# Kernel tuning notes

Hardware: AMD Instinct MI355X
Metric: run time of the kernel (lower is better)

The kernel has to match this reference:

```python
import jax, jax.numpy as jnp
import numpy as np

BLOCK = 256
H, D = 16, 128          # num_attention_heads, head_dim
HID = 2048              # hidden_size (= H*D)
FFN = 2048              # intermediate_size
E, TOPK = 8, 2          # num_local_experts, num_experts_per_tok
EPS_LN = 1e-5           # rms_norm_eps for layer norms
EPS_ATTN = float(np.finfo(np.float32).eps)  # torch RMSNorm default eps


def rmsnorm(x, w, eps):
    v = jnp.mean(jnp.square(x), axis=-1, keepdims=True)
    return x * jax.lax.rsqrt(v + eps) * w


def lightning_attn(x, slope, qkv_w, gate_w, norm_w, out_w):
    # x: [B,N,HID]; slope: [H,1,1]
    B, N, _ = x.shape
    qkv = jax.nn.silu(x @ qkv_w.T).reshape(B, N, H, 3 * D)
    q, k, v = jnp.split(qkv, 3, axis=-1)
    q = q.transpose(0, 2, 1, 3)  # [B,H,N,D]
    k = k.transpose(0, 2, 1, 3)
    v = v.transpose(0, 2, 1, 3)

    NB = N // BLOCK
    ar = jnp.arange(BLOCK, dtype=jnp.float32) + 1.0
    q_decay = jnp.exp(-slope * ar[:, None])             # [H,BLOCK,1]
    k_decay = jnp.exp(-slope * (BLOCK - ar[:, None]))   # [H,BLOCK,1]
    idx = ar[:, None] - ar[None, :]                      # [BLOCK,BLOCK]
    diag_decay = jnp.exp(jnp.where(idx >= 0, -(slope * idx), -jnp.inf))  # [H,BLOCK,BLOCK]
    block_decay = jnp.exp(-slope * BLOCK)                # [H,1,1]

    qb = q.reshape(B, H, NB, BLOCK, D).transpose(2, 0, 1, 3, 4)  # [NB,B,H,BLOCK,D]
    kb = k.reshape(B, H, NB, BLOCK, D).transpose(2, 0, 1, 3, 4)
    vb = v.reshape(B, H, NB, BLOCK, D).transpose(2, 0, 1, 3, 4)

    def step(kv, blk):
        qi, ki, vi = blk                                   # [B,H,BLOCK,D]
        o_nd = jnp.einsum('bhmd,bhde->bhme', qi * q_decay, kv)
        qk = jnp.einsum('bhmd,bhnd->bhmn', qi, ki) * diag_decay[None]
        o_d = jnp.einsum('bhmn,bhne->bhme', qk, vi)
        kv = block_decay * kv + jnp.einsum('bhmd,bhme->bhde', ki * k_decay, vi)
        return kv, o_nd + o_d

    kv0 = jnp.zeros((B, H, D, D), jnp.float32)
    _, out = jax.lax.scan(step, kv0, (qb, kb, vb))         # out: [NB,B,H,BLOCK,D]
    out = out.transpose(1, 2, 0, 3, 4).reshape(B, H, N, D)
    out = out.transpose(0, 2, 1, 3).reshape(B, N, H * D)   # b h n d -> b n (h d)
    out = rmsnorm(out, norm_w, EPS_ATTN)
    out = jax.nn.sigmoid(x @ gate_w.T) * out
    return out @ out_w.T


def moe(x, router_w, w1, w2, w3):
    # x: [B,N,HID]
    B, N, _ = x.shape
    xt = x.reshape(B * N, HID)                             # [T,HID]
    T = B * N
    logits = xt @ router_w.T                               # [T,E]
    probs = jax.nn.softmax(logits.astype(jnp.float32), axis=-1)
    w, sel = jax.lax.top_k(probs, TOPK)                    # [T,TOPK]
    w = w / jnp.sum(w, axis=-1, keepdims=True)
    w = w.astype(xt.dtype)
    # dense combine weights [T,E] (top-k experts are distinct)
    cw = jnp.zeros((T, E), xt.dtype).at[jnp.arange(T)[:, None], sel].add(w)
    h1 = jax.nn.silu(jnp.einsum('td,efd->tef', xt, w1))    # [T,E,FFN]
    h3 = jnp.einsum('td,efd->tef', xt, w3)
    ye = jnp.einsum('tef,edf->ted', h1 * h3, w2)           # [T,E,HID]
    out = jnp.einsum('te,ted->td', cw, ye)
    return out.reshape(B, N, HID)


def setup_inputs() -> dict:
    key = jax.random.key(0)
    ks = jax.random.split(key, 12)
    s = 0.02
    B, N = 1, 1024
    x = jax.random.normal(ks[0], (B, N, HID), jnp.float32)
    # ALiBi-like positive per-head decay rates
    slope_rate = (1.0 / (2.0 ** (8.0 * (jnp.arange(H, dtype=jnp.float32) + 1) / H))).reshape(H, 1, 1)
    return {
        'x': x,
        'slope_rate': slope_rate,
        'ln1_w': jnp.ones((HID,), jnp.float32),
        'ln2_w': jnp.ones((HID,), jnp.float32),
        'qkv_w': jax.random.normal(ks[1], (3 * H * D, HID), jnp.float32) * s,
        'ogate_w': jax.random.normal(ks[2], (H * D, HID), jnp.float32) * s,
        'anorm_w': jnp.ones((H * D,), jnp.float32),
        'aout_w': jax.random.normal(ks[3], (HID, H * D), jnp.float32) * s,
        'router_w': jax.random.normal(ks[4], (E, HID), jnp.float32) * s,
        'w1': jax.random.normal(ks[5], (E, FFN, HID), jnp.float32) * s,
        'w2': jax.random.normal(ks[6], (E, HID, FFN), jnp.float32) * s,
        'w3': jax.random.normal(ks[7], (E, FFN, HID), jnp.float32) * s,
    }


def reference(x, slope_rate, ln1_w, ln2_w, qkv_w, ogate_w, anorm_w, aout_w, router_w, w1, w2, w3):
    # pre-norm residual decoder layer (alpha=beta=1, postnorm=False, no shared MoE)
    r = x
    h = rmsnorm(x, ln1_w, EPS_LN)
    h = r + lightning_attn(h, slope_rate, qkv_w, ogate_w, anorm_w, aout_w)
    r = h
    h2 = rmsnorm(h, ln2_w, EPS_LN)
    return r + moe(h2, router_w, w1, w2, w3)
```

## Files before the change

kernel.cpp:

```cpp
#include <hip/hip_runtime.h>
#include <math.h>

#define NTOK 1024
#define NHID 2048
#define NQKV 6144
#define NHEADS 16
#define DHEAD 128
#define ABLK 256
#define NEXPERT 8
#define NFFN 2048
#define EPS_LN 1e-5f
#define EPS_ATTN 1.1920929e-7f

typedef __bf16 bf8v __attribute__((ext_vector_type(8)));
typedef __bf16 bf4v __attribute__((ext_vector_type(4)));
typedef float f4v __attribute__((ext_vector_type(4)));

static __device__ __forceinline__ f4v mfma16(bf8v a, bf8v b, f4v c) {
  return __builtin_amdgcn_mfma_f32_16x16x32_bf16(a, b, c, 0, 0, 0);
}

static __device__ __forceinline__ void gl2lds16(const void* g, void* l) {
  __builtin_amdgcn_global_load_lds(
      (const __attribute__((address_space(1))) unsigned int*)g,
      (__attribute__((address_space(3))) unsigned int*)l, 16, 0, 0);
}

__global__ __launch_bounds__(256) void rms_kernel(const float* __restrict__ in,
                                                  const float* __restrict__ w,
                                                  __bf16* __restrict__ out_bf,
                                                  const float* __restrict__ gate,
                                                  float* __restrict__ copy_out,
                                                  float* __restrict__ out_f32,
                                                  float eps) {
  const int row = blockIdx.x, tid = threadIdx.x;
  const float* p = in + (size_t)row * NHID;
  float4 v0 = *(const float4*)(p + 4 * tid);
  float4 v1 = *(const float4*)(p + 1024 + 4 * tid);
  float ss = v0.x * v0.x + v0.y * v0.y + v0.z * v0.z + v0.w * v0.w
           + v1.x * v1.x + v1.y * v1.y + v1.z * v1.z + v1.w * v1.w;
  for (int off = 32; off > 0; off >>= 1) ss += __shfl_down(ss, off);
  __shared__ float red[4];
  const int wv = tid >> 6, ln = tid & 63;
  if (ln == 0) red[wv] = ss;
  __syncthreads();
  const float tot = red[0] + red[1] + red[2] + red[3];
  const float rinv = rsqrtf(tot * (1.f / NHID) + eps);
  float4 w0 = *(const float4*)(w + 4 * tid);
  float4 w1 = *(const float4*)(w + 1024 + 4 * tid);
  float4 o0, o1;
  o0.x = v0.x * rinv * w0.x; o0.y = v0.y * rinv * w0.y;
  o0.z = v0.z * rinv * w0.z; o0.w = v0.w * rinv * w0.w;
  o1.x = v1.x * rinv * w1.x; o1.y = v1.y * rinv * w1.y;
  o1.z = v1.z * rinv * w1.z; o1.w = v1.w * rinv * w1.w;
  if (gate) {
    const float* gp = gate + (size_t)row * NHID;
    float4 g0 = *(const float4*)(gp + 4 * tid);
    float4 g1 = *(const float4*)(gp + 1024 + 4 * tid);
    o0.x *= g0.x; o0.y *= g0.y; o0.z *= g0.z; o0.w *= g0.w;
    o1.x *= g1.x; o1.y *= g1.y; o1.z *= g1.z; o1.w *= g1.w;
  }
  bf4v b0, b1;
  b0[0] = (__bf16)o0.x; b0[1] = (__bf16)o0.y; b0[2] = (__bf16)o0.z; b0[3] = (__bf16)o0.w;
  b1[0] = (__bf16)o1.x; b1[1] = (__bf16)o1.y; b1[2] = (__bf16)o1.z; b1[3] = (__bf16)o1.w;
  *(bf4v*)(out_bf + (size_t)row * NHID + 4 * tid) = b0;
  *(bf4v*)(out_bf + (size_t)row * NHID + 1024 + 4 * tid) = b1;
  if (out_f32) {
    *(float4*)(out_f32 + (size_t)row * NHID + 4 * tid) = o0;
    *(float4*)(out_f32 + (size_t)row * NHID + 1024 + 4 * tid) = o1;
  }
  if (copy_out) {
    *(float4*)(copy_out + (size_t)row * NHID + 4 * tid) = v0;
    *(float4*)(copy_out + (size_t)row * NHID + 1024 + 4 * tid) = v1;
  }
}

enum { GM_QKV = 0, GM_GATE = 1, GM_AOUT = 2, GM_MOE1 = 3, GM_MOE3 = 4, GM_MOE2 = 5 };

struct GArgs {
  const __bf16* A; const float* B; void* C;
  const float* res;
  __bf16* q_s; __bf16* k_s; __bf16* v_s;
  const int* perm; const int* segoff; const float* pw;
  float* outp;
  int N, K;
};

template <int MODE>
__global__ __launch_bounds__(256, 3) void gemm_bt(GArgs g) {
  const int n0 = blockIdx.x * 64;
  const int m0 = blockIdx.y * 128;
  int segbase = 0, cnt = 0x40000000, e = 0;
  if constexpr (MODE >= GM_MOE1) {
    e = blockIdx.z;
    segbase = g.segoff[e];
    cnt = g.segoff[e + 1] - segbase;
    if (m0 >= cnt) return;
  }
  const float* Bp = g.B + (size_t)e * g.N * g.K + (size_t)n0 * g.K;
  __shared__ __bf16 As[3][128 * 32] __attribute__((aligned(16)));
  __shared__ float Bs[3][64 * 32] __attribute__((aligned(16)));
  const int tid = threadIdx.x;
  const int w = tid >> 6, lane = tid & 63;
  const int wm = (w >> 1) * 64, wn = (w & 1) * 32;
  const int lm = lane & 15, quad = lane >> 4;
  const int K = g.K;

  const __bf16* aptr[2];
#pragma unroll
  for (int qi = 0; qi < 2; qi++) {
    const int r = w * 32 + qi * 16 + (lane >> 2);
    const int m = m0 + r;
    long grow;
    if constexpr (MODE == GM_MOE1 || MODE == GM_MOE3) {
      int mm = m < cnt ? m : cnt - 1;
      grow = g.perm[segbase + mm];
    } else if constexpr (MODE == GM_MOE2) {
      grow = segbase + (m < cnt ? m : cnt - 1);
    } else {
      grow = m;
    }
    const int gc = (lane & 3) ^ (r & 3);
    aptr[qi] = g.A + (size_t)grow * K + gc * 8;
  }
  const float* bptr[2];
  {
    const int lr = lane >> 3;
    const int coff = ((lane & 7) ^ lr) * 4;
#pragma unroll
    for (int qi = 0; qi < 2; qi++) {
      const int r = (w * 2 + qi) * 8 + lr;
      bptr[qi] = Bp + (size_t)r * K + coff;
    }
  }

  const f4v fz = {0.f, 0.f, 0.f, 0.f};
  f4v acc[4][2];
#pragma unroll
  for (int i = 0; i < 4; i++) {
    acc[i][0] = fz; acc[i][1] = fz;
  }

  const int KT = K >> 5;

#define STAGE(tt, bb)                                      \
  do {                                                     \
    const int kk_ = (tt) << 5;                             \
    gl2lds16(aptr[0] + kk_, &As[bb][(w * 32) * 32]);       \
    gl2lds16(aptr[1] + kk_, &As[bb][(w * 32 + 16) * 32]);  \
    gl2lds16(bptr[0] + kk_, &Bs[bb][(w * 16) * 32]);       \
    gl2lds16(bptr[1] + kk_, &Bs[bb][(w * 16 + 8) * 32]);   \
  } while (0)

  STAGE(0, 0);
  STAGE(1, 1);

  const int swa = lm & 3;
  const int swb = lm & 7;
  for (int t = 0; t < KT; ++t) {
    const int cur = t % 3;
    if (t + 1 < KT) {
      asm volatile("s_waitcnt vmcnt(4)" ::: "memory");
    } else {
      asm volatile("s_waitcnt vmcnt(0)" ::: "memory");
    }
    __builtin_amdgcn_s_barrier();
    if (t + 2 < KT) {
      const int nb = (t + 2) % 3;
      STAGE(t + 2, nb);
    }
    bf8v af[4], bfv[2];
#pragma unroll
    for (int i = 0; i < 4; i++) {
      const int ra = wm + i * 16 + lm;
      af[i] = *(const bf8v*)&As[cur][ra * 32 + ((quad ^ swa) << 3)];
    }
#pragma unroll
    for (int j = 0; j < 2; j++) {
      const int rb = wn + j * 16 + lm;
      const float4 x0 = *(const float4*)&Bs[cur][rb * 32 + (((quad * 2) ^ swb) << 2)];
      const float4 x1 = *(const float4*)&Bs[cur][rb * 32 + (((quad * 2 + 1) ^ swb) << 2)];
      bf8v t8;
      t8[0] = (__bf16)x0.x; t8[1] = (__bf16)x0.y; t8[2] = (__bf16)x0.z; t8[3] = (__bf16)x0.w;
      t8[4] = (__bf16)x1.x; t8[5] = (__bf16)x1.y; t8[6] = (__bf16)x1.z; t8[7] = (__bf16)x1.w;
      bfv[j] = t8;
    }
#pragma unroll
    for (int i = 0; i < 4; i++)
#pragma unroll
      for (int j = 0; j < 2; j++) acc[i][j] = mfma16(af[i], bfv[j], acc[i][j]);
  }
#undef STAGE

#pragma unroll
  for (int i = 0; i < 4; i++) {
#pragma unroll
    for (int r = 0; r < 4; r++) {
      const int m = m0 + wm + i * 16 + quad * 4 + r;
      int tok = 0;
      float wgt = 0.f;
      if constexpr (MODE == GM_MOE2) {
        if (m < cnt) { tok = g.perm[segbase + m]; wgt = g.pw[segbase + m]; }
      }
#pragma unroll
      for (int j = 0; j < 2; j++) {
        const int col = n0 + wn + j * 16 + lm;
        float v = acc[i][j][r];
        if constexpr (MODE == GM_QKV) {
          v = v / (1.f + expf(-v));
          int head = col / 384;
          int rem = col - head * 384;
          int which = rem >> 7;
          int d = rem & 127;
          __bf16* dst = which == 0 ? g.q_s : (which == 1 ? g.k_s : g.v_s);
          dst[((size_t)head * NTOK + m) * DHEAD + d] = (__bf16)v;
        } else if constexpr (MODE == GM_GATE) {
          ((float*)g.C)[(size_t)m * g.N + col] = 1.f / (1.f + expf(-v));
        } else if constexpr (MODE == GM_AOUT) {
          ((float*)g.C)[(size_t)m * g.N + col] = v + g.res[(size_t)m * g.N + col];
        } else if constexpr (MODE == GM_MOE1) {
          if (m < cnt)
            ((__bf16*)g.C)[(size_t)(segbase + m) * g.N + col] = (__bf16)(v / (1.f + expf(-v)));
        } else if constexpr (MODE == GM_MOE3) {
          if (m < cnt) {
            size_t ix = (size_t)(segbase + m) * g.N + col;
            __bf16* tc = (__bf16*)g.C;
            tc[ix] = (__bf16)(v * (float)tc[ix]);
          }
        } else if constexpr (MODE == GM_MOE2) {
          if (m < cnt) atomicAdd(&g.outp[(size_t)tok * NHID + col], wgt * v);
        }
      }
    }
  }
}

__global__ __launch_bounds__(512) void attn_pass1(const __bf16* __restrict__ k_s,
                                                  const __bf16* __restrict__ v_s,
                                                  const float* __restrict__ slope,
                                                  float* __restrict__ S) {
  const int h = blockIdx.x >> 2, b = blockIdx.x & 3;
  const float s = slope[h];
  __shared__ __bf16 kT[128][40] __attribute__((aligned(16)));
  __shared__ __bf16 vT[128][40] __attribute__((aligned(16)));
  const int tid = threadIdx.x, wave = tid >> 6, lane = tid & 63;
  const int lm = lane & 15, quad = lane >> 4;
  const __bf16* kb = k_s + ((size_t)h * NTOK + b * ABLK) * DHEAD;
  const __bf16* vb = v_s + ((size_t)h * NTOK + b * ABLK) * DHEAD;
  const int sd = tid & 127, sg = (tid >> 7) * 8;
  const f4v fz = {0.f, 0.f, 0.f, 0.f};
  f4v acc[8];
#pragma unroll
  for (int j = 0; j < 8; j++) acc[j] = fz;
  for (int ic = 0; ic < 8; ic++) {
    __syncthreads();
    bf8v kq, vq;
#pragma unroll
    for (int ii = 0; ii < 8; ii++) {
      int ig = ic * 32 + sg + ii;
      float kd = expf(-s * (float)(ABLK - 1 - ig));
      kq[ii] = (__bf16)((float)kb[(size_t)ig * DHEAD + sd] * kd);
      vq[ii] = vb[(size_t)ig * DHEAD + sd];
    }
    *(bf8v*)&kT[sd][sg] = kq;
    *(bf8v*)&vT[sd][sg] = vq;
    __syncthreads();
    bf8v a = *(const bf8v*)&kT[wave * 16 + lm][quad * 8];
#pragma unroll
    for (int j = 0; j < 8; j++) {
      bf8v bb = *(const bf8v*)&vT[j * 16 + lm][quad * 8];
      acc[j] = mfma16(a, bb, acc[j]);
    }
  }
  float* Sp = S + (size_t)(h * 4 + b) * (128 * 128);
#pragma unroll
  for (int j = 0; j < 8; j++)
#pragma unroll
    for (int r = 0; r < 4; r++)
      Sp[(size_t)(wave * 16 + quad * 4 + r) * 128 + j * 16 + lm] = acc[j][r];
}

__global__ __launch_bounds__(512) void attn_pass2(const __bf16* __restrict__ q_s,
                                                  const __bf16* __restrict__ k_s,
                                                  const __bf16* __restrict__ v_s,
                                                  const float* __restrict__ slope,
                                                  const float* __restrict__ S,
                                                  float* __restrict__ attn_raw) {
  const int h = blockIdx.x >> 2, b = blockIdx.x & 3;
  const float s = slope[h];
  __shared__ __bf16 kvb[128][136] __attribute__((aligned(16)));
  __shared__ __bf16 vT[128][40] __attribute__((aligned(16)));
  __shared__ __bf16 ki[32][136] __attribute__((aligned(16)));
  __shared__ __bf16 qkb[256][40] __attribute__((aligned(16)));
  const int tid = threadIdx.x, w = tid >> 6, lane = tid & 63;
  const int lm = lane & 15, quad = lane >> 4;
  {
    const int sd = tid >> 2;
    const int e0 = (tid & 3) * 32;
    float vals[32];
#pragma unroll
    for (int u = 0; u < 32; u++) vals[u] = 0.f;
    for (int j = 0; j < b; j++) {
      float c = expf(-s * 256.f * (float)(b - 1 - j));
      const float* Sp = S + (size_t)(h * 4 + j) * (128 * 128) + (size_t)sd * 128 + e0;
#pragma unroll
      for (int u4 = 0; u4 < 8; u4++) {
        float4 sv = *(const float4*)(Sp + u4 * 4);
        vals[u4 * 4 + 0] += c * sv.x; vals[u4 * 4 + 1] += c * sv.y;
        vals[u4 * 4 + 2] += c * sv.z; vals[u4 * 4 + 3] += c * sv.w;
      }
    }
#pragma unroll
    for (int u = 0; u < 32; u++) kvb[e0 + u][sd] = (__bf16)vals[u];
  }
  __syncthreads();
  const __bf16* qb = q_s + ((size_t)h * NTOK + b * ABLK) * DHEAD;
  const __bf16* kb = k_s + ((size_t)h * NTOK + b * ABLK) * DHEAD;
  const __bf16* vb = v_s + ((size_t)h * NTOK + b * ABLK) * DHEAD;
  bf8v aq[2][4];
#pragma unroll
  for (int mf = 0; mf < 2; mf++) {
    const int m = w * 32 + mf * 16 + lm;
#pragma unroll
    for (int kc = 0; kc < 4; kc++)
      aq[mf][kc] = *(const bf8v*)(qb + (size_t)m * DHEAD + kc * 32 + quad * 8);
  }
  const f4v fz = {0.f, 0.f, 0.f, 0.f};
  f4v accO[2][8];
#pragma unroll
  for (int mf = 0; mf < 2; mf++)
#pragma unroll
    for (int nf = 0; nf < 8; nf++) accO[mf][nf] = fz;
#pragma unroll
  for (int kc = 0; kc < 4; kc++) {
#pragma unroll
    for (int nf = 0; nf < 8; nf++) {
      bf8v bb = *(const bf8v*)&kvb[nf * 16 + lm][kc * 32 + quad * 8];
      accO[0][nf] = mfma16(aq[0][kc], bb, accO[0][nf]);
      accO[1][nf] = mfma16(aq[1][kc], bb, accO[1][nf]);
    }
  }
#pragma unroll
  for (int mf = 0; mf < 2; mf++) {
#pragma unroll
    for (int r = 0; r < 4; r++) {
      const int m = w * 32 + mf * 16 + quad * 4 + r;
      const float qd = expf(-s * (float)(m + 1));
#pragma unroll
      for (int nf = 0; nf < 8; nf++) accO[mf][nf][r] *= qd;
    }
  }
  for (int ic = 0; ic < 8; ic++) {
    __syncthreads();
    {
      const int si = tid >> 4, dc = (tid & 15) * 8;
      *(bf8v*)&ki[si][dc] = *(const bf8v*)(kb + (size_t)(ic * 32 + si) * DHEAD + dc);
    }
    {
      const int se = tid & 127, sg = (tid >> 7) * 8;
      bf8v t;
#pragma unroll
      for (int ii = 0; ii < 8; ii++)
        t[ii] = vb[(size_t)(ic * 32 + sg + ii) * DHEAD + se];
      *(bf8v*)&vT[se][sg] = t;
    }
    __syncthreads();
    f4v acc2[2][2];
    acc2[0][0] = fz; acc2[0][1] = fz; acc2[1][0] = fz; acc2[1][1] = fz;
#pragma unroll
    for (int kc = 0; kc < 4; kc++) {
#pragma unroll
      for (int f = 0; f < 2; f++) {
        bf8v bk = *(const bf8v*)&ki[f * 16 + lm][kc * 32 + quad * 8];
        acc2[0][f] = mfma16(aq[0][kc], bk, acc2[0][f]);
        acc2[1][f] = mfma16(aq[1][kc], bk, acc2[1][f]);
      }
    }
#pragma unroll
    for (int mf = 0; mf < 2; mf++) {
#pragma unroll
      for (int f = 0; f < 2; f++) {
#pragma unroll
        for (int r = 0; r < 4; r++) {
          const int m = w * 32 + mf * 16 + quad * 4 + r;
          const int i = ic * 32 + f * 16 + lm;
          float v = acc2[mf][f][r];
          v = (m >= i) ? v * expf(-s * (float)(m - i)) : 0.f;
          qkb[m][f * 16 + lm] = (__bf16)v;
        }
      }
    }
    __syncthreads();
#pragma unroll
    for (int mf = 0; mf < 2; mf++) {
      bf8v aqk = *(const bf8v*)&qkb[w * 32 + mf * 16 + lm][quad * 8];
#pragma unroll
      for (int nf = 0; nf < 8; nf++) {
        bf8v bv = *(const bf8v*)&vT[nf * 16 + lm][quad * 8];
        accO[mf][nf] = mfma16(aqk, bv, accO[mf][nf]);
      }
    }
  }
  float* op = attn_raw + (size_t)(b * ABLK) * NHID + h * DHEAD;
#pragma unroll
  for (int mf = 0; mf < 2; mf++)
#pragma unroll
    for (int r = 0; r < 4; r++) {
      const int m = w * 32 + mf * 16 + quad * 4 + r;
#pragma unroll
      for (int nf = 0; nf < 8; nf++)
        op[(size_t)m * NHID + nf * 16 + lm] = accO[mf][nf][r];
    }
}

__global__ __launch_bounds__(256) void router_kernel(const float* __restrict__ h2,
                                                     const float* __restrict__ rw,
                                                     int* __restrict__ eidx,
                                                     float* __restrict__ ew) {
  const int wave = threadIdx.x >> 6, lane = threadIdx.x & 63;
  const int t = blockIdx.x * 4 + wave;
  float a[8];
#pragma unroll
  for (int e = 0; e < 8; e++) a[e] = 0.f;
  for (int d = lane; d < NHID; d += 64) {
    float xv = h2[(size_t)t * NHID + d];
#pragma unroll
    for (int e = 0; e < 8; e++) a[e] += xv * rw[(size_t)e * NHID + d];
  }
#pragma unroll
  for (int e = 0; e < 8; e++)
    for (int off = 32; off > 0; off >>= 1) a[e] += __shfl_down(a[e], off);
  if (lane == 0) {
    int i1 = 0;
#pragma unroll
    for (int e = 1; e < 8; e++)
      if (a[e] > a[i1]) i1 = e;
    int i2 = i1 == 0 ? 1 : 0;
#pragma unroll
    for (int e = 0; e < 8; e++) {
      if (e == i1 || e == i2) continue;
      if (a[e] > a[i2]) i2 = e;
    }
    float be = expf(a[i2] - a[i1]);
    float w1 = 1.f / (1.f + be), w2 = be / (1.f + be);
    eidx[2 * t] = i1; eidx[2 * t + 1] = i2;
    ew[2 * t] = w1; ew[2 * t + 1] = w2;
  }
}

__global__ __launch_bounds__(256) void build_lists(const int* __restrict__ eidx,
                                                   const float* __restrict__ ew,
                                                   int* __restrict__ segoff,
                                                   int* __restrict__ perm,
                                                   float* __restrict__ pw) {
  __shared__ int cnt[8], cur[8], offs[9];
  const int tid = threadIdx.x;
  if (tid < 8) cnt[tid] = 0;
  __syncthreads();
  for (int t = tid; t < NTOK; t += 256) {
    atomicAdd(&cnt[eidx[2 * t]], 1);
    atomicAdd(&cnt[eidx[2 * t + 1]], 1);
  }
  __syncthreads();
  if (tid == 0) {
    int o = 0;
    for (int e = 0; e < 8; e++) { offs[e] = o; o += cnt[e]; }
    offs[8] = o;
    for (int e = 0; e < 9; e++) segoff[e] = offs[e];
  }
  __syncthreads();
  if (tid < 8) cur[tid] = offs[tid];
  __syncthreads();
  for (int t = tid; t < NTOK; t += 256) {
    for (int k = 0; k < 2; k++) {
      int e = eidx[2 * t + k];
      int pos = atomicAdd(&cur[e], 1);
      perm[pos] = t;
      pw[pos] = ew[2 * t + k];
    }
  }
}

extern "C" void kernel_launch(void* const* d_in, const int* in_sizes, int n_in,
                              void* d_out, int out_size, void* d_ws, size_t ws_size,
                              hipStream_t stream) {
  (void)in_sizes; (void)n_in; (void)out_size; (void)ws_size;
  const float* x        = (const float*)d_in[0];
  const float* slope    = (const float*)d_in[1];
  const float* ln1_w    = (const float*)d_in[2];
  const float* ln2_w    = (const float*)d_in[3];
  const float* qkv_w    = (const float*)d_in[4];
  const float* ogate_w  = (const float*)d_in[5];
  const float* anorm_w  = (const float*)d_in[6];
  const float* aout_w   = (const float*)d_in[7];
  const float* router_w = (const float*)d_in[8];
  const float* w1       = (const float*)d_in[9];
  const float* w2       = (const float*)d_in[10];
  const float* w3       = (const float*)d_in[11];
  float* out = (float*)d_out;
  float* ws  = (float*)d_ws;

  const size_t MW = (size_t)NTOK * NHID;
  __bf16* a_ln   = (__bf16*)ws;
  __bf16* q_s    = (__bf16*)(ws + MW);
  __bf16* k_s    = (__bf16*)(ws + 2 * MW);
  __bf16* v_s    = (__bf16*)(ws + 3 * MW);
  float* Sbuf    = ws + 4 * MW;
  float* attn_raw = ws + 4 * MW + MW / 2;
  float* gatebuf  = ws + 5 * MW + MW / 2;
  __bf16* t1     = (__bf16*)attn_raw;
  float* h2f     = gatebuf;
  float* rbase   = ws + 6 * MW + MW / 2;
  int*   eidx   = (int*)rbase;
  float* ew     = rbase + 2048;
  int*   segoff = (int*)(rbase + 4096);
  int*   perm   = (int*)(rbase + 4112);
  float* pw     = rbase + 6160;
  float* h_res  = ws + 2 * MW;
  __bf16* h2    = v_s;
  __bf16* ag    = a_ln;

  rms_kernel<<<dim3(NTOK), dim3(256), 0, stream>>>(x, ln1_w, a_ln, nullptr, nullptr, nullptr, EPS_LN);
  {
    GArgs g{}; g.A = a_ln; g.B = qkv_w; g.q_s = q_s; g.k_s = k_s; g.v_s = v_s;
    g.N = NQKV; g.K = NHID;
    gemm_bt<GM_QKV><<<dim3(NQKV / 64, NTOK / 128), dim3(256), 0, stream>>>(g);
  }
  attn_pass1<<<dim3(64), dim3(512), 0, stream>>>(k_s, v_s, slope, Sbuf);
  attn_pass2<<<dim3(64), dim3(512), 0, stream>>>(q_s, k_s, v_s, slope, Sbuf, attn_raw);
  {
    GArgs g{}; g.A = a_ln; g.B = ogate_w; g.C = gatebuf; g.N = NHID; g.K = NHID;
    gemm_bt<GM_GATE><<<dim3(32, 8), dim3(256), 0, stream>>>(g);
  }
  rms_kernel<<<dim3(NTOK), dim3(256), 0, stream>>>(attn_raw, anorm_w, ag, gatebuf, nullptr, nullptr, EPS_ATTN);
  {
    GArgs g{}; g.A = ag; g.B = aout_w; g.C = h_res; g.res = x; g.N = NHID; g.K = NHID;
    gemm_bt<GM_AOUT><<<dim3(32, 8), dim3(256), 0, stream>>>(g);
  }
  rms_kernel<<<dim3(NTOK), dim3(256), 0, stream>>>(h_res, ln2_w, h2, nullptr, out, h2f, EPS_LN);
  router_kernel<<<dim3(NTOK / 4), dim3(256), 0, stream>>>(h2f, router_w, eidx, ew);
  build_lists<<<dim3(1), dim3(256), 0, stream>>>(eidx, ew, segoff, perm, pw);
  {
    GArgs g{}; g.A = h2; g.B = w1; g.C = t1; g.perm = perm; g.segoff = segoff;
    g.N = NFFN; g.K = NHID;
    gemm_bt<GM_MOE1><<<dim3(32, 16, 8), dim3(256), 0, stream>>>(g);
  }
  {
    GArgs g{}; g.A = h2; g.B = w3; g.C = t1; g.perm = perm; g.segoff = segoff;
    g.N = NFFN; g.K = NHID;
    gemm_bt<GM_MOE3><<<dim3(32, 16, 8), dim3(256), 0, stream>>>(g);
  }
  {
    GArgs g{}; g.A = t1; g.B = w2; g.outp = out; g.perm = perm; g.segoff = segoff; g.pw = pw;
    g.N = NHID; g.K = NFFN;
    gemm_bt<GM_MOE2><<<dim3(32, 16, 8), dim3(256), 0, stream>>>(g);
  }
}
```

Measured before the change: 824.7 us.

## Fuse MoE w1/w3 GEMMs into dual-B kernel and halve M tile for square GEMMs

Merges the two MoE up-projection GEMMs (w1 and w3) into one kernel that shares the gathered A tile and keeps two accumulator sets, applying silu(x1)*x3 in the epilogue. This avoids loading the activations twice and avoids the read-modify-write of the intermediate buffer. It also shrinks the M tile to 64 rows for the gate and attention-output GEMMs, doubling their grid and raising the occupancy hint, to fill more CUs. The fused kernel uses more registers and LDS, so its occupancy drops to 2 blocks.

```diff
diff --git a/kernel.cpp b/kernel.cpp
--- a/kernel.cpp
+++ b/kernel.cpp
@@ -75,10 +75,10 @@
   }
 }
 
-enum { GM_QKV = 0, GM_GATE = 1, GM_AOUT = 2, GM_MOE1 = 3, GM_MOE3 = 4, GM_MOE2 = 5 };
+enum { GM_QKV = 0, GM_GATE = 1, GM_AOUT = 2, GM_MOE13 = 3, GM_MOE2 = 4 };
 
 struct GArgs {
-  const __bf16* A; const float* B; void* C;
+  const __bf16* A; const float* B; const float* B3; void* C;
   const float* res;
   __bf16* q_s; __bf16* k_s; __bf16* v_s;
   const int* perm; const int* segoff; const float* pw;
@@ -87,32 +87,44 @@
 };
 
 template <int MODE>
-__global__ __launch_bounds__(256, 3) void gemm_bt(GArgs g) {
+__global__ __launch_bounds__(256, (MODE == GM_GATE || MODE == GM_AOUT) ? 4
+                                  : (MODE == GM_MOE13 ? 2 : 3))
+void gemm_bt(GArgs g) {
+  constexpr int MR = (MODE == GM_GATE || MODE == GM_AOUT) ? 64 : 128;
+  constexpr bool DUAL = (MODE == GM_MOE13);
+  constexpr int MI = MR / 32;
+  constexpr int LW = MR / 64 + 2 + (DUAL ? 2 : 0);
+
   const int n0 = blockIdx.x * 64;
-  const int m0 = blockIdx.y * 128;
+  const int m0 = blockIdx.y * MR;
   int segbase = 0, cnt = 0x40000000, e = 0;
-  if constexpr (MODE >= GM_MOE1) {
+  if constexpr (MODE >= GM_MOE13) {
     e = blockIdx.z;
     segbase = g.segoff[e];
     cnt = g.segoff[e + 1] - segbase;
     if (m0 >= cnt) return;
   }
   const float* Bp = g.B + (size_t)e * g.N * g.K + (size_t)n0 * g.K;
-  __shared__ __bf16 As[3][128 * 32] __attribute__((aligned(16)));
+  const float* Bp3 = nullptr;
+  if constexpr (DUAL) Bp3 = g.B3 + (size_t)e * g.N * g.K + (size_t)n0 * g.K;
+
+  __shared__ __bf16 As[3][MR * 32] __attribute__((aligned(16)));
   __shared__ float Bs[3][64 * 32] __attribute__((aligned(16)));
+  __shared__ float B3s[DUAL ? 3 : 1][DUAL ? 64 * 32 : 1] __attribute__((aligned(16)));
+
   const int tid = threadIdx.x;
   const int w = tid >> 6, lane = tid & 63;
-  const int wm = (w >> 1) * 64, wn = (w & 1) * 32;
+  const int wm = (w >> 1) * (MR / 2), wn = (w & 1) * 32;
   const int lm = lane & 15, quad = lane >> 4;
   const int K = g.K;
 
-  const __bf16* aptr[2];
-#pragma unroll
-  for (int qi = 0; qi < 2; qi++) {
-    const int r = w * 32 + qi * 16 + (lane >> 2);
+  const __bf16* aptr[MR / 64];
+#pragma unroll
+  for (int qi = 0; qi < MR / 64; qi++) {
+    const int r = w * (MR / 4) + qi * 16 + (lane >> 2);
     const int m = m0 + r;
     long grow;
-    if constexpr (MODE == GM_MOE1 || MODE == GM_MOE3) {
+    if constexpr (MODE == GM_MOE13) {
       int mm = m < cnt ? m : cnt - 1;
       grow = g.perm[segbase + mm];
     } else if constexpr (MODE == GM_MOE2) {
@@ -124,6 +136,7 @@
     aptr[qi] = g.A + (size_t)grow * K + gc * 8;
   }
   const float* bptr[2];
+  const float* b3ptr[2] = {nullptr, nullptr};
   {
     const int lr = lane >> 3;
     const int coff = ((lane & 7) ^ lr) * 4;
@@ -131,25 +144,33 @@
     for (int qi = 0; qi < 2; qi++) {
       const int r = (w * 2 + qi) * 8 + lr;
       bptr[qi] = Bp + (size_t)r * K + coff;
+      if constexpr (DUAL) b3ptr[qi] = Bp3 + (size_t)r * K + coff;
     }
   }
 
   const f4v fz = {0.f, 0.f, 0.f, 0.f};
-  f4v acc[4][2];
-#pragma unroll
-  for (int i = 0; i < 4; i++) {
+  f4v acc[MI][2];
+  f4v acc3[DUAL ? MI : 1][2];
+#pragma unroll
+  for (int i = 0; i < MI; i++) {
     acc[i][0] = fz; acc[i][1] = fz;
+    if constexpr (DUAL) { acc3[i][0] = fz; acc3[i][1] = fz; }
   }
 
   const int KT = K >> 5;
 
-#define STAGE(tt, bb)                                      \
-  do {                                                     \
-    const int kk_ = (tt) << 5;                             \
-    gl2lds16(aptr[0] + kk_, &As[bb][(w * 32) * 32]);       \
-    gl2lds16(aptr[1] + kk_, &As[bb][(w * 32 + 16) * 32]);  \
-    gl2lds16(bptr[0] + kk_, &Bs[bb][(w * 16) * 32]);       \
-    gl2lds16(bptr[1] + kk_, &Bs[bb][(w * 16 + 8) * 32]);   \
+#define STAGE(tt, bb)                                                     \
+  do {                                                                    \
+    const int kk_ = (tt) << 5;                                            \
+    _Pragma("unroll")                                                     \
+    for (int qi = 0; qi < MR / 64; qi++)                                  \
+      gl2lds16(aptr[qi] + kk_, &As[bb][(w * (MR / 4) + qi * 16) * 32]);   \
+    gl2lds16(bptr[0] + kk_, &Bs[bb][(w * 16) * 32]);                      \
+    gl2lds16(bptr[1] + kk_, &Bs[bb][(w * 16 + 8) * 32]);                  \
+    if constexpr (DUAL) {                                                 \
+      gl2lds16(b3ptr[0] + kk_, &B3s[bb][(w * 16) * 32]);                  \
+      gl2lds16(b3ptr[1] + kk_, &B3s[bb][(w * 16 + 8) * 32]);              \
+    }                                                                     \
   } while (0)
 
   STAGE(0, 0);
@@ -160,18 +181,17 @@
   for (int t = 0; t < KT; ++t) {
     const int cur = t % 3;
     if (t + 1 < KT) {
-      asm volatile("s_waitcnt vmcnt(4)" ::: "memory");
+      if constexpr (LW == 3)      asm volatile("s_waitcnt vmcnt(3)" ::: "memory");
+      else if constexpr (LW == 4) asm volatile("s_waitcnt vmcnt(4)" ::: "memory");
+      else                        asm volatile("s_waitcnt vmcnt(6)" ::: "memory");
     } else {
       asm volatile("s_waitcnt vmcnt(0)" ::: "memory");
     }
     __builtin_amdgcn_s_barrier();
-    if (t + 2 < KT) {
-      const int nb = (t + 2) % 3;
-      STAGE(t + 2, nb);
-    }
-    bf8v af[4], bfv[2];
-#pragma unroll
-    for (int i = 0; i < 4; i++) {
+    if (t + 2 < KT) STAGE(t + 2, (t + 2) % 3);
+    bf8v af[MI], bfv[2];
+#pragma unroll
+    for (int i = 0; i < MI; i++) {
       const int ra = wm + i * 16 + lm;
       af[i] = *(const bf8v*)&As[cur][ra * 32 + ((quad ^ swa) << 3)];
     }
@@ -186,14 +206,31 @@
       bfv[j] = t8;
     }
 #pragma unroll
-    for (int i = 0; i < 4; i++)
+    for (int i = 0; i < MI; i++)
 #pragma unroll
       for (int j = 0; j < 2; j++) acc[i][j] = mfma16(af[i], bfv[j], acc[i][j]);
+    if constexpr (DUAL) {
+      bf8v b3v[2];
+#pragma unroll
+      for (int j = 0; j < 2; j++) {
+        const int rb = wn + j * 16 + lm;
+        const float4 x0 = *(const float4*)&B3s[cur][rb * 32 + (((quad * 2) ^ swb) << 2)];
+        const float4 x1 = *(const float4*)&B3s[cur][rb * 32 + (((quad * 2 + 1) ^ swb) << 2)];
+        bf8v t8;
+        t8[0] = (__bf16)x0.x; t8[1] = (__bf16)x0.y; t8[2] = (__bf16)x0.z; t8[3] = (__bf16)x0.w;
+        t8[4] = (__bf16)x1.x; t8[5] = (__bf16)x1.y; t8[6] = (__bf16)x1.z; t8[7] = (__bf16)x1.w;
+        b3v[j] = t8;
+      }
+#pragma unroll
+      for (int i = 0; i < MI; i++)
+#pragma unroll
+        for (int j = 0; j < 2; j++) acc3[i][j] = mfma16(af[i], b3v[j], acc3[i][j]);
+    }
   }
 #undef STAGE
 
 #pragma unroll
-  for (int i = 0; i < 4; i++) {
+  for (int i = 0; i < MI; i++) {
 #pragma unroll
     for (int r = 0; r < 4; r++) {
       const int m = m0 + wm + i * 16 + quad * 4 + r;
@@ -218,14 +255,10 @@
           ((float*)g.C)[(size_t)m * g.N + col] = 1.f / (1.f + expf(-v));
         } else if constexpr (MODE == GM_AOUT) {
           ((float*)g.C)[(size_t)m * g.N + col] = v + g.res[(size_t)m * g.N + col];
-        } else if constexpr (MODE == GM_MOE1) {
-          if (m < cnt)
-            ((__bf16*)g.C)[(size_t)(segbase + m) * g.N + col] = (__bf16)(v / (1.f + expf(-v)));
-        } else if constexpr (MODE == GM_MOE3) {
+        } else if constexpr (MODE == GM_MOE13) {
           if (m < cnt) {
-            size_t ix = (size_t)(segbase + m) * g.N + col;
-            __bf16* tc = (__bf16*)g.C;
-            tc[ix] = (__bf16)(v * (float)tc[ix]);
+            float s1 = v / (1.f + expf(-v));
+            ((__bf16*)g.C)[(size_t)(segbase + m) * g.N + col] = (__bf16)(s1 * acc3[i][j][r]);
           }
         } else if constexpr (MODE == GM_MOE2) {
           if (m < cnt) atomicAdd(&g.outp[(size_t)tok * NHID + col], wgt * v);
@@ -530,25 +563,20 @@
   attn_pass2<<<dim3(64), dim3(512), 0, stream>>>(q_s, k_s, v_s, slope, Sbuf, attn_raw);
   {
     GArgs g{}; g.A = a_ln; g.B = ogate_w; g.C = gatebuf; g.N = NHID; g.K = NHID;
-    gemm_bt<GM_GATE><<<dim3(32, 8), dim3(256), 0, stream>>>(g);
+    gemm_bt<GM_GATE><<<dim3(32, 16), dim3(256), 0, stream>>>(g);
   }
   rms_kernel<<<dim3(NTOK), dim3(256), 0, stream>>>(attn_raw, anorm_w, ag, gatebuf, nullptr, nullptr, EPS_ATTN);
   {
     GArgs g{}; g.A = ag; g.B = aout_w; g.C = h_res; g.res = x; g.N = NHID; g.K = NHID;
-    gemm_bt<GM_AOUT><<<dim3(32, 8), dim3(256), 0, stream>>>(g);
+    gemm_bt<GM_AOUT><<<dim3(32, 16), dim3(256), 0, stream>>>(g);
   }
   rms_kernel<<<dim3(NTOK), dim3(256), 0, stream>>>(h_res, ln2_w, h2, nullptr, out, h2f, EPS_LN);
   router_kernel<<<dim3(NTOK / 4), dim3(256), 0, stream>>>(h2f, router_w, eidx, ew);
   build_lists<<<dim3(1), dim3(256), 0, stream>>>(eidx, ew, segoff, perm, pw);
   {
-    GArgs g{}; g.A = h2; g.B = w1; g.C = t1; g.perm = perm; g.segoff = segoff;
+    GArgs g{}; g.A = h2; g.B = w1; g.B3 = w3; g.C = t1; g.perm = perm; g.segoff = segoff;
     g.N = NFFN; g.K = NHID;
-    gemm_bt<GM_MOE1><<<dim3(32, 16, 8), dim3(256), 0, stream>>>(g);
-  }
-  {
-    GArgs g{}; g.A = h2; g.B = w3; g.C = t1; g.perm = perm; g.segoff = segoff;
-    g.N = NFFN; g.K = NHID;
-    gemm_bt<GM_MOE3><<<dim3(32, 16, 8), dim3(256), 0, stream>>>(g);
+    gemm_bt<GM_MOE13><<<dim3(32, 16, 8), dim3(256), 0, stream>>>(g);
   }
   {
     GArgs g{}; g.A = t1; g.B = w2; g.outp = out; g.perm = perm; g.segoff = segoff; g.pw = pw;
```

New measurement: 817.5 us. About the same (-0.9%).
